# Kernel tuning notes

Measured on AMD Instinct MI355X. Metric: run time of the kernel, lower is better.

The kernel has to match this reference:

```python
import jax, jax.numpy as jnp
import numpy as np

B, L, H, E, D = 2, 2048, 8, 64, 64


def setup_inputs() -> dict:
    key = jax.random.key(0)
    k0, k1, k2, k3 = jax.random.split(key, 4)
    u = jax.random.normal(k0, (B, L, H, D), dtype=jnp.float32)
    q = jax.random.normal(k1, (B, L, H, E), dtype=jnp.float32)
    k = jax.random.normal(k2, (B, L, H, E), dtype=jnp.float32)
    v = jax.random.normal(k3, (B, L, H, D), dtype=jnp.float32)
    # causal mask: True where attention is DISALLOWED (strict upper triangle)
    attn_mask = jnp.triu(jnp.ones((L, L), dtype=bool), k=1)[None, None]  # (1,1,L,L)
    return {"u": u, "q": q, "k": k, "v": v, "attn_mask": attn_mask}


def reference(u, q, k, v, attn_mask):
    # q,k: [B,L,H,E]; v,u: [B,L,H,D]; attn_mask: [1,1,L,S] bool (True = masked)
    Edim = q.shape[-1]
    S = k.shape[1]
    scale = 1.0 / np.sqrt(Edim)
    scores = jnp.einsum('blhe,bshe->bhls', q, k)  # [B,H,L,S]
    x = jax.nn.relu(scale * scores)
    # attention_normalize(method='squared_relu'): relu(x)^2 / seq_len; masked -> 0
    A = jnp.where(attn_mask, 0.0, x * x) / S  # [B,H,L,S]
    # dropout is identity in eval mode
    V = u * jnp.einsum('bhls,bshd->blhd', A, v)  # [B,L,H,D]
    return V
```

## Files before the change

### kernel.cpp

```cpp
#include <hip/hip_runtime.h>
#include <hip/hip_bf16.h>

namespace {
constexpr int Lc = 2048, Hc = 8;
constexpr int RS = Hc * 64;
constexpr int NKT = 32;
constexpr int TILE_BYTES = 16384;
}

typedef __attribute__((ext_vector_type(8))) short bf16x8;
typedef __attribute__((ext_vector_type(16))) float f32x16;
typedef unsigned int u32;
typedef __attribute__((ext_vector_type(4))) u32 u32x4;

__device__ __forceinline__ u32 bfu(float x) {
    return (u32)__builtin_bit_cast(unsigned short, __float2bfloat16(x));
}
__device__ __forceinline__ short f2bf(float x) {
    return (short)__builtin_bit_cast(unsigned short, __float2bfloat16(x));
}

#define MFMA32(a, b, c) __builtin_amdgcn_mfma_f32_32x32x16_bf16((a), (b), (c), 0, 0, 0)

#define GLL16(gp, lp) __builtin_amdgcn_global_load_lds( \
    (const __attribute__((address_space(1))) unsigned int*)(gp), \
    (__attribute__((address_space(3))) unsigned int*)(lp), 16, 0, 0)

__global__ __launch_bounds__(256)
void prep_kv(const float* __restrict__ kg, const float* __restrict__ vg,
             short* __restrict__ ws)
{
    const int kt = blockIdx.x, bh = blockIdx.y;
    const int b = bh >> 3, h = bh & 7;
    const size_t base = ((size_t)b * Lc * Hc + h) * 64;
    char* tile = (char*)ws + (size_t)(bh * NKT + kt) * TILE_BYTES;
    const int tid = threadIdx.x;

    {
        const int c = tid & 7, e0 = c * 8;
        #pragma unroll
        for (int p = 0; p < 2; ++p) {
            const int s = (tid >> 3) + 32 * p;
            const float* src = kg + base + (size_t)(kt * 64 + s) * RS + e0;
            float4 x0 = *(const float4*)src;
            float4 x1 = *(const float4*)(src + 4);
            bf16x8 w = { f2bf(x0.x), f2bf(x0.y), f2bf(x0.z), f2bf(x0.w),
                         f2bf(x1.x), f2bf(x1.y), f2bf(x1.z), f2bf(x1.w) };
            const int lane = (c & 1) * 32 + (s & 31);
            const int byte = ((s >> 5) * 4 + (c >> 1)) * 1024 + lane * 16;
            *(bf16x8*)(tile + byte) = w;
        }
    }
    {
        const int d = tid & 63;
        #pragma unroll
        for (int p = 0; p < 2; ++p) {
            const int sblk = (tid >> 6) + 4 * p;
            const int s0 = sblk * 8;
            float xv[8];
            #pragma unroll
            for (int j = 0; j < 8; ++j)
                xv[j] = vg[base + (size_t)(kt * 64 + s0 + j) * RS + d];
            bf16x8 w = { f2bf(xv[0]), f2bf(xv[1]), f2bf(xv[2]), f2bf(xv[3]),
                         f2bf(xv[4]), f2bf(xv[5]), f2bf(xv[6]), f2bf(xv[7]) };
            const int lane = (sblk & 1) * 32 + (d & 31);
            const int byte = 8192 + ((d >> 5) * 4 + (sblk >> 1)) * 1024 + lane * 16;
            *(bf16x8*)(tile + byte) = w;
        }
    }
}

__global__ __launch_bounds__(256, 1)
void gate_attn(const float* __restrict__ ug, const float* __restrict__ qg,
               const short* __restrict__ ws, float* __restrict__ outg)
{
    __shared__ __align__(16) char lds[2][4 * 8192];

    const int tid = threadIdx.x;
    const int ktp = tid >> 6, lane = tid & 63;
    const int col = lane & 31, hi = lane >> 5;

    const int pr = blockIdx.x, bh = blockIdx.y;
    const int b = bh >> 3, h = bh & 7;
    const size_t base = ((size_t)b * Lc * Hc + h) * 64;
    const char* wsbh = (const char*)ws + (size_t)bh * NKT * TILE_BYTES;

    auto STAGEG = [&](int t0, int buf, int smax) {
        #pragma unroll
        for (int t = 0; t < 4; ++t) {
            const int kt2 = t0 + t;
            if (kt2 <= smax) {
                const char* src = wsbh + (size_t)kt2 * TILE_BYTES + tid * 16;
                char* dst = &lds[buf][t * 8192] + tid * 16;
                GLL16(src, dst);
                GLL16(src + 4096, dst + 4096);
            }
        }
    };

    auto RUN_STRIP = [&](int strip) {
        const int IT = (strip + 4) >> 2;

        bf16x8 qf[2][4];
        #pragma unroll
        for (int q2 = 0; q2 < 2; ++q2)
            #pragma unroll
            for (int es = 0; es < 4; ++es) {
                const float* p = qg + base +
                    (size_t)(strip * 64 + q2 * 32 + col) * RS + es * 16 + hi * 8;
                float4 a = *(const float4*)p;
                float4 c2 = *(const float4*)(p + 4);
                qf[q2][es] = (bf16x8){ f2bf(a.x),  f2bf(a.y),  f2bf(a.z),  f2bf(a.w),
                                       f2bf(c2.x), f2bf(c2.y), f2bf(c2.z), f2bf(c2.w) };
            }

        f32x16 oacc[2][2];
        #pragma unroll
        for (int q2 = 0; q2 < 2; ++q2)
            #pragma unroll
            for (int r = 0; r < 16; ++r) { oacc[q2][0][r] = 0.f; oacc[q2][1][r] = 0.f; }

        STAGEG(0, 0, strip);
        __syncthreads();

        for (int it = 0; it < IT; ++it) {
            if (it + 1 < IT) STAGEG(4 * (it + 1), (it & 1) ^ 1, strip);
            const int kt = 4 * it + ktp;
            if (kt <= strip) {
                const char* vsrc = wsbh + (size_t)kt * TILE_BYTES + 8192 + lane * 16;
                bf16x8 vf[2][4];
                #pragma unroll
                for (int dh = 0; dh < 2; ++dh)
                    #pragma unroll
                    for (int ks = 0; ks < 4; ++ks)
                        vf[dh][ks] = *(const bf16x8*)(vsrc + (dh * 4 + ks) * 1024);

                const char* kb = &lds[it & 1][ktp * 8192];
                const bool dmask = (kt == strip);
                u32 pa[2][4][4];

                #pragma unroll
                for (int sb = 0; sb < 2; ++sb) {
                    f32x16 sacc0 = (f32x16)(0.f), sacc1 = (f32x16)(0.f);
                    #pragma unroll
                    for (int es = 0; es < 4; ++es) {
                        bf16x8 kf = *(const bf16x8*)(kb + (sb * 4 + es) * 1024 + lane * 16);
                        sacc0 = MFMA32(kf, qf[0][es], sacc0);
                        sacc1 = MFMA32(kf, qf[1][es], sacc1);
                    }
                    #pragma unroll
                    for (int q2 = 0; q2 < 2; ++q2) {
                        const f32x16& sv = q2 ? sacc1 : sacc0;
                        const int qg2 = strip * 64 + q2 * 32 + col;
                        float pv[16];
                        #pragma unroll
                        for (int r = 0; r < 16; ++r) {
                            float x = sv[r];
                            x = (x > 0.f) ? x * x : 0.f;
                            const int s_g = kt * 64 + sb * 32 + (r & 3) + 8 * (r >> 2) + 4 * hi;
                            if (dmask && s_g > qg2) x = 0.f;
                            pv[r] = x;
                        }
                        u32 W[8];
                        #pragma unroll
                        for (int t = 0; t < 8; ++t)
                            W[t] = bfu(pv[2 * t]) | (bfu(pv[2 * t + 1]) << 16);
                        asm volatile("v_permlane32_swap_b32 %0, %1" : "+v"(W[0]), "+v"(W[2]));
                        asm volatile("v_permlane32_swap_b32 %0, %1" : "+v"(W[1]), "+v"(W[3]));
                        asm volatile("v_permlane32_swap_b32 %0, %1" : "+v"(W[4]), "+v"(W[6]));
                        asm volatile("v_permlane32_swap_b32 %0, %1" : "+v"(W[5]), "+v"(W[7]));
                        pa[q2][sb * 2 + 0][0] = W[0]; pa[q2][sb * 2 + 0][1] = W[1];
                        pa[q2][sb * 2 + 0][2] = W[2]; pa[q2][sb * 2 + 0][3] = W[3];
                        pa[q2][sb * 2 + 1][0] = W[4]; pa[q2][sb * 2 + 1][1] = W[5];
                        pa[q2][sb * 2 + 1][2] = W[6]; pa[q2][sb * 2 + 1][3] = W[7];
                    }
                }

                #pragma unroll
                for (int dh = 0; dh < 2; ++dh)
                    #pragma unroll
                    for (int ks = 0; ks < 4; ++ks) {
                        u32x4 p0 = { pa[0][ks][0], pa[0][ks][1], pa[0][ks][2], pa[0][ks][3] };
                        u32x4 p1 = { pa[1][ks][0], pa[1][ks][1], pa[1][ks][2], pa[1][ks][3] };
                        oacc[0][dh] = MFMA32(__builtin_bit_cast(bf16x8, p0), vf[dh][ks], oacc[0][dh]);
                        oacc[1][dh] = MFMA32(__builtin_bit_cast(bf16x8, p1), vf[dh][ks], oacc[1][dh]);
                    }
            }
            __syncthreads();
        }

        float* red = (float*)&lds[0][0];
        #pragma unroll
        for (int q2 = 0; q2 < 2; ++q2)
            #pragma unroll
            for (int dh = 0; dh < 2; ++dh)
                #pragma unroll
                for (int r = 0; r < 16; ++r) {
                    const int m = q2 * 32 + (r & 3) + 8 * (r >> 2) + 4 * hi;
                    red[(ktp * 64 + m) * 64 + dh * 32 + col] = oacc[q2][dh][r];
                }
        __syncthreads();

        const float sc = 1.0f / (64.0f * 2048.0f);
        #pragma unroll
        for (int j = 0; j < 4; ++j) {
            const int e = tid + 256 * j;
            const int row = e >> 4, c4 = (e & 15) * 4;
            float4 s = make_float4(0.f, 0.f, 0.f, 0.f);
            #pragma unroll
            for (int k = 0; k < 4; ++k) {
                const float4 p = *(const float4*)&red[(k * 64 + row) * 64 + c4];
                s.x += p.x; s.y += p.y; s.z += p.z; s.w += p.w;
            }
            const size_t idx = base + (size_t)(strip * 64 + row) * RS + c4;
            const float4 uu = *(const float4*)&ug[idx];
            float4 o;
            o.x = uu.x * s.x * sc; o.y = uu.y * s.y * sc;
            o.z = uu.z * s.z * sc; o.w = uu.w * s.w * sc;
            *(float4*)&outg[idx] = o;
        }
        __syncthreads();
    };

    RUN_STRIP(31 - pr);
    RUN_STRIP(pr);
}

extern "C" void kernel_launch(void* const* d_in, const int* in_sizes, int n_in,
                              void* d_out, int out_size, void* d_ws, size_t ws_size,
                              hipStream_t stream) {
    const float* u = (const float*)d_in[0];
    const float* q = (const float*)d_in[1];
    const float* k = (const float*)d_in[2];
    const float* v = (const float*)d_in[3];
    float* out = (float*)d_out;

    prep_kv<<<dim3(NKT, 16), dim3(256), 0, stream>>>(k, v, (short*)d_ws);
    gate_attn<<<dim3(16, 16), dim3(256), 0, stream>>>(u, q, (const short*)d_ws, out);
}
```

Before: 41.81 us.

## Split attention into single-wave split-K blocks with atomic output accumulation

Replaces the 256-block, 4-wave kernel that staged K tiles through LDS and reduced partial sums in shared memory. It now launches 2048 single-wave blocks, each covering one query strip and up to 8 key tiles, mapped so that each XCD handles two batch-heads. Partial results are gated by u and added into a pre-zeroed output with float atomics, which needs an extra zeroing kernel. The bf16 packing now uses v_cvt_pk_bf16_f32, and K is read straight from global memory rather than through LDS. The goal is more parallelism and better load balance across the causal triangle, paid for with atomic traffic, nondeterministic summation order and an extra launch.

Result: slower. 66.18 us (+58.3%).

```diff
diff --git a/kernel.cpp b/kernel.cpp
--- a/kernel.cpp
+++ b/kernel.cpp
@@ -6,6 +6,7 @@
 constexpr int RS = Hc * 64;
 constexpr int NKT = 32;
 constexpr int TILE_BYTES = 16384;
+constexpr int OUT4 = 2 * Lc * Hc * 64 / 4;
 }
 
 typedef __attribute__((ext_vector_type(8))) short bf16x8;
@@ -13,18 +14,16 @@
 typedef unsigned int u32;
 typedef __attribute__((ext_vector_type(4))) u32 u32x4;
 
-__device__ __forceinline__ u32 bfu(float x) {
-    return (u32)__builtin_bit_cast(unsigned short, __float2bfloat16(x));
-}
 __device__ __forceinline__ short f2bf(float x) {
     return (short)__builtin_bit_cast(unsigned short, __float2bfloat16(x));
 }
 
 #define MFMA32(a, b, c) __builtin_amdgcn_mfma_f32_32x32x16_bf16((a), (b), (c), 0, 0, 0)
 
-#define GLL16(gp, lp) __builtin_amdgcn_global_load_lds( \
-    (const __attribute__((address_space(1))) unsigned int*)(gp), \
-    (__attribute__((address_space(3))) unsigned int*)(lp), 16, 0, 0)
+__global__ __launch_bounds__(256) void zero_out(float4* __restrict__ o) {
+    const int i = blockIdx.x * 256 + threadIdx.x;
+    if (i < OUT4) o[i] = make_float4(0.f, 0.f, 0.f, 0.f);
+}
 
 __global__ __launch_bounds__(256)
 void prep_kv(const float* __restrict__ kg, const float* __restrict__ vg,
@@ -70,160 +69,122 @@
     }
 }
 
-__global__ __launch_bounds__(256, 1)
+__global__ __launch_bounds__(64)
 void gate_attn(const float* __restrict__ ug, const float* __restrict__ qg,
                const short* __restrict__ ws, float* __restrict__ outg)
 {
-    __shared__ __align__(16) char lds[2][4 * 8192];
-
-    const int tid = threadIdx.x;
-    const int ktp = tid >> 6, lane = tid & 63;
+    const int gid = (int)blockIdx.x;
+    const int xcd = gid & 7;
+    const int uu = gid >> 3;
+    const int ktq = uu & 3;
+    const int z = uu >> 2;
+    const int sr = z & 31, bh_bit = z >> 5;
+    const int strip = (sr & 1) ? (31 - (sr >> 1)) : (sr >> 1);
+    const int bh = 2 * xcd + bh_bit;
+
+    const int kt0 = ktq * 8;
+    if (kt0 > strip) return;
+    const int kt1 = min(kt0 + 8, strip + 1);
+
+    const int lane = threadIdx.x;
     const int col = lane & 31, hi = lane >> 5;
-
-    const int pr = blockIdx.x, bh = blockIdx.y;
     const int b = bh >> 3, h = bh & 7;
     const size_t base = ((size_t)b * Lc * Hc + h) * 64;
     const char* wsbh = (const char*)ws + (size_t)bh * NKT * TILE_BYTES;
 
-    auto STAGEG = [&](int t0, int buf, int smax) {
-        #pragma unroll
-        for (int t = 0; t < 4; ++t) {
-            const int kt2 = t0 + t;
-            if (kt2 <= smax) {
-                const char* src = wsbh + (size_t)kt2 * TILE_BYTES + tid * 16;
-                char* dst = &lds[buf][t * 8192] + tid * 16;
-                GLL16(src, dst);
-                GLL16(src + 4096, dst + 4096);
-            }
-        }
-    };
-
-    auto RUN_STRIP = [&](int strip) {
-        const int IT = (strip + 4) >> 2;
-
-        bf16x8 qf[2][4];
-        #pragma unroll
-        for (int q2 = 0; q2 < 2; ++q2)
+    bf16x8 qf[2][4];
+    #pragma unroll
+    for (int q2 = 0; q2 < 2; ++q2)
+        #pragma unroll
+        for (int es = 0; es < 4; ++es) {
+            const float* p = qg + base +
+                (size_t)(strip * 64 + q2 * 32 + col) * RS + es * 16 + hi * 8;
+            float4 a = *(const float4*)p;
+            float4 c2 = *(const float4*)(p + 4);
+            qf[q2][es] = (bf16x8){ f2bf(a.x),  f2bf(a.y),  f2bf(a.z),  f2bf(a.w),
+                                   f2bf(c2.x), f2bf(c2.y), f2bf(c2.z), f2bf(c2.w) };
+        }
+
+    f32x16 oacc[2][2];
+    #pragma unroll
+    for (int q2 = 0; q2 < 2; ++q2)
+        #pragma unroll
+        for (int r = 0; r < 16; ++r) { oacc[q2][0][r] = 0.f; oacc[q2][1][r] = 0.f; }
+
+    for (int kt = kt0; kt < kt1; ++kt) {
+        const char* kb = wsbh + (size_t)kt * TILE_BYTES + lane * 16;
+
+        const char* vb = kb + 8192;
+        bf16x8 vf[2][4];
+        #pragma unroll
+        for (int dh = 0; dh < 2; ++dh)
+            #pragma unroll
+            for (int ks = 0; ks < 4; ++ks)
+                vf[dh][ks] = *(const bf16x8*)(vb + (dh * 4 + ks) * 1024);
+
+        const bool dmask = (kt == strip);
+        u32 pa[2][4][4];
+
+        #pragma unroll
+        for (int sb = 0; sb < 2; ++sb) {
+            f32x16 sacc0 = (f32x16)(0.f), sacc1 = (f32x16)(0.f);
             #pragma unroll
             for (int es = 0; es < 4; ++es) {
-                const float* p = qg + base +
-                    (size_t)(strip * 64 + q2 * 32 + col) * RS + es * 16 + hi * 8;
-                float4 a = *(const float4*)p;
-                float4 c2 = *(const float4*)(p + 4);
-                qf[q2][es] = (bf16x8){ f2bf(a.x),  f2bf(a.y),  f2bf(a.z),  f2bf(a.w),
-                                       f2bf(c2.x), f2bf(c2.y), f2bf(c2.z), f2bf(c2.w) };
-            }
-
-        f32x16 oacc[2][2];
-        #pragma unroll
-        for (int q2 = 0; q2 < 2; ++q2)
-            #pragma unroll
-            for (int r = 0; r < 16; ++r) { oacc[q2][0][r] = 0.f; oacc[q2][1][r] = 0.f; }
-
-        STAGEG(0, 0, strip);
-        __syncthreads();
-
-        for (int it = 0; it < IT; ++it) {
-            if (it + 1 < IT) STAGEG(4 * (it + 1), (it & 1) ^ 1, strip);
-            const int kt = 4 * it + ktp;
-            if (kt <= strip) {
-                const char* vsrc = wsbh + (size_t)kt * TILE_BYTES + 8192 + lane * 16;
-                bf16x8 vf[2][4];
-                #pragma unroll
-                for (int dh = 0; dh < 2; ++dh)
-                    #pragma unroll
-                    for (int ks = 0; ks < 4; ++ks)
-                        vf[dh][ks] = *(const bf16x8*)(vsrc + (dh * 4 + ks) * 1024);
-
-                const char* kb = &lds[it & 1][ktp * 8192];
-                const bool dmask = (kt == strip);
-                u32 pa[2][4][4];
-
-                #pragma unroll
-                for (int sb = 0; sb < 2; ++sb) {
-                    f32x16 sacc0 = (f32x16)(0.f), sacc1 = (f32x16)(0.f);
-                    #pragma unroll
-                    for (int es = 0; es < 4; ++es) {
-                        bf16x8 kf = *(const bf16x8*)(kb + (sb * 4 + es) * 1024 + lane * 16);
-                        sacc0 = MFMA32(kf, qf[0][es], sacc0);
-                        sacc1 = MFMA32(kf, qf[1][es], sacc1);
-                    }
-                    #pragma unroll
-                    for (int q2 = 0; q2 < 2; ++q2) {
-                        const f32x16& sv = q2 ? sacc1 : sacc0;
-                        const int qg2 = strip * 64 + q2 * 32 + col;
-                        float pv[16];
-                        #pragma unroll
-                        for (int r = 0; r < 16; ++r) {
-                            float x = sv[r];
-                            x = (x > 0.f) ? x * x : 0.f;
-                            const int s_g = kt * 64 + sb * 32 + (r & 3) + 8 * (r >> 2) + 4 * hi;
-                            if (dmask && s_g > qg2) x = 0.f;
-                            pv[r] = x;
-                        }
-                        u32 W[8];
-                        #pragma unroll
-                        for (int t = 0; t < 8; ++t)
-                            W[t] = bfu(pv[2 * t]) | (bfu(pv[2 * t + 1]) << 16);
-                        asm volatile("v_permlane32_swap_b32 %0, %1" : "+v"(W[0]), "+v"(W[2]));
-                        asm volatile("v_permlane32_swap_b32 %0, %1" : "+v"(W[1]), "+v"(W[3]));
-                        asm volatile("v_permlane32_swap_b32 %0, %1" : "+v"(W[4]), "+v"(W[6]));
-                        asm volatile("v_permlane32_swap_b32 %0, %1" : "+v"(W[5]), "+v"(W[7]));
-                        pa[q2][sb * 2 + 0][0] = W[0]; pa[q2][sb * 2 + 0][1] = W[1];
-                        pa[q2][sb * 2 + 0][2] = W[2]; pa[q2][sb * 2 + 0][3] = W[3];
-                        pa[q2][sb * 2 + 1][0] = W[4]; pa[q2][sb * 2 + 1][1] = W[5];
-                        pa[q2][sb * 2 + 1][2] = W[6]; pa[q2][sb * 2 + 1][3] = W[7];
-                    }
-                }
-
-                #pragma unroll
-                for (int dh = 0; dh < 2; ++dh)
-                    #pragma unroll
-                    for (int ks = 0; ks < 4; ++ks) {
-                        u32x4 p0 = { pa[0][ks][0], pa[0][ks][1], pa[0][ks][2], pa[0][ks][3] };
-                        u32x4 p1 = { pa[1][ks][0], pa[1][ks][1], pa[1][ks][2], pa[1][ks][3] };
-                        oacc[0][dh] = MFMA32(__builtin_bit_cast(bf16x8, p0), vf[dh][ks], oacc[0][dh]);
-                        oacc[1][dh] = MFMA32(__builtin_bit_cast(bf16x8, p1), vf[dh][ks], oacc[1][dh]);
-                    }
-            }
-            __syncthreads();
-        }
-
-        float* red = (float*)&lds[0][0];
-        #pragma unroll
-        for (int q2 = 0; q2 < 2; ++q2)
-            #pragma unroll
-            for (int dh = 0; dh < 2; ++dh)
+                bf16x8 kf = *(const bf16x8*)(kb + (sb * 4 + es) * 1024);
+                sacc0 = MFMA32(kf, qf[0][es], sacc0);
+                sacc1 = MFMA32(kf, qf[1][es], sacc1);
+            }
+            #pragma unroll
+            for (int q2 = 0; q2 < 2; ++q2) {
+                const f32x16& sv = q2 ? sacc1 : sacc0;
+                const int qg2 = strip * 64 + q2 * 32 + col;
+                float pv[16];
                 #pragma unroll
                 for (int r = 0; r < 16; ++r) {
-                    const int m = q2 * 32 + (r & 3) + 8 * (r >> 2) + 4 * hi;
-                    red[(ktp * 64 + m) * 64 + dh * 32 + col] = oacc[q2][dh][r];
+                    float x = sv[r];
+                    x = (x > 0.f) ? x * x : 0.f;
+                    const int s_g = kt * 64 + sb * 32 + (r & 3) + 8 * (r >> 2) + 4 * hi;
+                    if (dmask && s_g > qg2) x = 0.f;
+                    pv[r] = x;
                 }
-        __syncthreads();
-
-        const float sc = 1.0f / (64.0f * 2048.0f);
-        #pragma unroll
-        for (int j = 0; j < 4; ++j) {
-            const int e = tid + 256 * j;
-            const int row = e >> 4, c4 = (e & 15) * 4;
-            float4 s = make_float4(0.f, 0.f, 0.f, 0.f);
-            #pragma unroll
-            for (int k = 0; k < 4; ++k) {
-                const float4 p = *(const float4*)&red[(k * 64 + row) * 64 + c4];
-                s.x += p.x; s.y += p.y; s.z += p.z; s.w += p.w;
-            }
-            const size_t idx = base + (size_t)(strip * 64 + row) * RS + c4;
-            const float4 uu = *(const float4*)&ug[idx];
-            float4 o;
-            o.x = uu.x * s.x * sc; o.y = uu.y * s.y * sc;
-            o.z = uu.z * s.z * sc; o.w = uu.w * s.w * sc;
-            *(float4*)&outg[idx] = o;
-        }
-        __syncthreads();
-    };
-
-    RUN_STRIP(31 - pr);
-    RUN_STRIP(pr);
+                u32 W[8];
+                #pragma unroll
+                for (int t = 0; t < 8; ++t)
+                    asm("v_cvt_pk_bf16_f32 %0, %1, %2"
+                        : "=v"(W[t]) : "v"(pv[2 * t]), "v"(pv[2 * t + 1]));
+                asm volatile("v_permlane32_swap_b32 %0, %1" : "+v"(W[0]), "+v"(W[2]));
+                asm volatile("v_permlane32_swap_b32 %0, %1" : "+v"(W[1]), "+v"(W[3]));
+                asm volatile("v_permlane32_swap_b32 %0, %1" : "+v"(W[4]), "+v"(W[6]));
+                asm volatile("v_permlane32_swap_b32 %0, %1" : "+v"(W[5]), "+v"(W[7]));
+                pa[q2][sb * 2 + 0][0] = W[0]; pa[q2][sb * 2 + 0][1] = W[1];
+                pa[q2][sb * 2 + 0][2] = W[2]; pa[q2][sb * 2 + 0][3] = W[3];
+                pa[q2][sb * 2 + 1][0] = W[4]; pa[q2][sb * 2 + 1][1] = W[5];
+                pa[q2][sb * 2 + 1][2] = W[6]; pa[q2][sb * 2 + 1][3] = W[7];
+            }
+        }
+
+        #pragma unroll
+        for (int dh = 0; dh < 2; ++dh)
+            #pragma unroll
+            for (int ks = 0; ks < 4; ++ks) {
+                u32x4 p0 = { pa[0][ks][0], pa[0][ks][1], pa[0][ks][2], pa[0][ks][3] };
+                u32x4 p1 = { pa[1][ks][0], pa[1][ks][1], pa[1][ks][2], pa[1][ks][3] };
+                oacc[0][dh] = MFMA32(__builtin_bit_cast(bf16x8, p0), vf[dh][ks], oacc[0][dh]);
+                oacc[1][dh] = MFMA32(__builtin_bit_cast(bf16x8, p1), vf[dh][ks], oacc[1][dh]);
+            }
+    }
+
+    const float sc = 1.0f / (64.0f * 2048.0f);
+    #pragma unroll
+    for (int q2 = 0; q2 < 2; ++q2)
+        #pragma unroll
+        for (int dh = 0; dh < 2; ++dh)
+            #pragma unroll
+            for (int r = 0; r < 16; ++r) {
+                const int m = q2 * 32 + (r & 3) + 8 * (r >> 2) + 4 * hi;
+                const size_t idx = base + (size_t)(strip * 64 + m) * RS + dh * 32 + col;
+                atomicAdd(&outg[idx], ug[idx] * oacc[q2][dh][r] * sc);
+            }
 }
 
 extern "C" void kernel_launch(void* const* d_in, const int* in_sizes, int n_in,
@@ -235,6 +196,7 @@
     const float* v = (const float*)d_in[3];
     float* out = (float*)d_out;
 
+    zero_out<<<dim3((OUT4 + 255) / 256), dim3(256), 0, stream>>>((float4*)out);
     prep_kv<<<dim3(NKT, 16), dim3(256), 0, stream>>>(k, v, (short*)d_ws);
-    gate_attn<<<dim3(16, 16), dim3(256), 0, stream>>>(u, q, (const short*)d_ws, out);
-}
+    gate_attn<<<dim3(2048), dim3(64), 0, stream>>>(u, q, (const short*)d_ws, out);
+}
```
